# Kernel optimization log

Measured on AMD Instinct MI355X. Metric: run time of the kernel, lower is better.

## Reference

```python
import jax, jax.numpy as jnp
import numpy as np
import math

B, S, D, H = 4, 2048, 1024, 16
HD = D // H  # head dim = 64


def setup_inputs() -> dict:
    key = jax.random.key(0)
    ks = jax.random.split(key, 8)
    queries = jax.random.normal(ks[0], (B, S, D), dtype=jnp.float32)
    keys = jax.random.normal(ks[1], (B, S, D), dtype=jnp.float32)
    values = jax.random.normal(ks[2], (B, S, D), dtype=jnp.float32)
    valid_lens = jnp.maximum(jax.random.randint(ks[3], (B,), 0, S), 1).astype(jnp.int64)
    scale = 1.0 / math.sqrt(D)
    Wq = jax.random.normal(ks[4], (H, D, HD), dtype=jnp.float32) * scale
    Wk = jax.random.normal(ks[5], (H, D, HD), dtype=jnp.float32) * scale
    Wv = jax.random.normal(ks[6], (H, D, HD), dtype=jnp.float32) * scale
    Wo = jax.random.normal(ks[7], (H * HD, D), dtype=jnp.float32) * scale
    return {"queries": queries, "keys": keys, "values": values,
            "valid_lens": valid_lens, "Wq": Wq, "Wk": Wk, "Wv": Wv, "Wo": Wo}


def reference(queries, keys, values, valid_lens, Wq, Wk, Wv, Wo):
    # Per-head projections, batched over heads: [B,S,D] x [H,D,HD] -> [B,H,S,HD]
    q = jnp.einsum('bsd,hde->bhse', queries, Wq)
    k = jnp.einsum('bsd,hde->bhse', keys, Wk)
    v = jnp.einsum('bsd,hde->bhse', values, Wv)
    # Scaled dot-product scores: [B,H,S,S]
    scores = jnp.einsum('bhse,bhte->bhst', q, k) / jnp.sqrt(jnp.float32(HD))
    # Padding mask only (causal=False default in the torch forward)
    pad = jnp.arange(S)[None, :] >= valid_lens[:, None]  # [B,S] True = masked
    scores = jnp.where(pad[:, None, None, :], -jnp.inf, scores)
    attn = jax.nn.softmax(scores, axis=-1)
    out = jnp.einsum('bhst,bhte->bhse', attn, v)  # [B,H,S,HD]
    out = out.transpose(0, 2, 1, 3).reshape(q.shape[0], S, H * HD)  # concat heads
    return out @ Wo
```

## Files before the change

### kernel.cpp

```cpp
#include <hip/hip_runtime.h>
#include <hip/hip_bf16.h>

typedef __bf16 bf16;
typedef __attribute__((ext_vector_type(8))) __bf16 bf16x8;
typedef __attribute__((ext_vector_type(4))) float f32x4;

#define DEV __device__ __forceinline__

DEV float fexp2(float x) {
#if __has_builtin(__builtin_amdgcn_exp2f)
  return __builtin_amdgcn_exp2f(x);
#else
  return exp2f(x);
#endif
}

DEV void gload_lds16(const void* g, void* l) {
  __builtin_amdgcn_global_load_lds(
      (__attribute__((address_space(1))) void*)(g),
      (__attribute__((address_space(3))) void*)(l), 16, 0, 0);
}

template <int N>
DEV void waitvm() { asm volatile("s_waitcnt vmcnt(%0)" ::"n"(N) : "memory"); }
DEV void fence() { asm volatile("" ::: "memory"); }
DEV void bar() { fence(); __builtin_amdgcn_s_barrier(); fence(); }

__global__ void k_cvt_act(const float* __restrict__ q, const float* __restrict__ k,
                          const float* __restrict__ v, bf16* __restrict__ qb,
                          bf16* __restrict__ kb, bf16* __restrict__ vb) {
  const int bid = blockIdx.x;
  const int which = bid >> 12;
  const float* in = which == 0 ? q : which == 1 ? k : v;
  bf16* out = which == 0 ? qb : which == 1 ? kb : vb;
  const int i = (bid & 4095) * 256 + threadIdx.x;
  const float4* p = reinterpret_cast<const float4*>(in) + (size_t)i * 2;
  float4 a = p[0], b = p[1];
  bf16x8 o;
  o[0] = (bf16)a.x; o[1] = (bf16)a.y; o[2] = (bf16)a.z; o[3] = (bf16)a.w;
  o[4] = (bf16)b.x; o[5] = (bf16)b.y; o[6] = (bf16)b.z; o[7] = (bf16)b.w;
  *reinterpret_cast<bf16x8*>(out + (size_t)i * 8) = o;
}

__global__ void k_cvt_w(const float* __restrict__ Wq, const float* __restrict__ Wk,
                        const float* __restrict__ Wv, const float* __restrict__ Wo,
                        bf16* __restrict__ WqkvT, bf16* __restrict__ WoT) {
  const int idx = blockIdx.x * blockDim.x + threadIdx.x;
  const int which = idx >> 20, r = idx & ((1 << 20) - 1);
  if (which < 3) {
    const float* W = which == 0 ? Wq : which == 1 ? Wk : Wv;
    const int d = r & 1023, n = r >> 10;
    float val = W[((size_t)(n >> 6) << 16) + (size_t)d * 64 + (n & 63)];
    if (which == 0) val *= 0.180336880f;
    WqkvT[((size_t)which << 20) + r] = (bf16)val;
  } else {
    const int kk = r & 1023, n = r >> 10;
    WoT[r] = (bf16)Wo[(size_t)kk * 1024 + n];
  }
}

DEV void stage_half(const bf16* __restrict__ srcb, bf16 (*lds)[64], int h, int k0,
                    int tid) {
  const int wv = tid >> 6;
#pragma unroll
  for (int l = 0; l < 2; ++l) {
    const int row = h * 128 + l * 64 + (tid >> 3);
    const int e = (((tid & 7) ^ (row & 7)) << 3);
    gload_lds16(srcb + (size_t)row * 1024 + k0 + e,
                (char*)&lds[h * 128 + l * 64][0] + wv * 1024);
  }
}

DEV bf16x8 ldsfrag(const bf16 (*lds)[64], int row, int kk, int lgrp) {
  const int ch = ((kk << 2) + lgrp) ^ (row & 7);
  return *reinterpret_cast<const bf16x8*>((const char*)&lds[row][0] + (ch << 4));
}

__global__ __launch_bounds__(512, 2) void k_gemm_qkv(const bf16* __restrict__ qA,
                                                     const bf16* __restrict__ kA,
                                                     const bf16* __restrict__ vA,
                                                     const bf16* __restrict__ Wt,
                                                     bf16* __restrict__ Qh,
                                                     bf16* __restrict__ Kh,
                                                     bf16* __restrict__ Vt) {
  __shared__ __align__(16) bf16 AsB[2][256][64];
  __shared__ __align__(16) bf16 BsB[2][256][64];
  const int tid = threadIdx.x, lane = tid & 63, w = tid >> 6;
  const int lgrp = lane >> 4, lid = lane & 15;
  const int wr = w >> 2, wn = w & 3;
  const int bid0 = blockIdx.x;
  const int bid = (bid0 & 7) * 48 + (bid0 >> 3);
  const int proj = bid >> 7;
  const int rem = bid & 127;
  const int mt = rem >> 2, ntl = rem & 3;
  const int m0 = mt * 256, n0 = ntl * 256;
  const bf16* A = proj == 0 ? qA : proj == 1 ? kA : vA;
  const bf16* Am = A + (size_t)m0 * 1024;
  const bf16* Bt = Wt + ((size_t)proj * 1024 + n0) * 1024;

  f32x4 acc[8][4] = {};
  constexpr int NT = 16;

  stage_half(Am, AsB[0], 0, 0, tid);
  stage_half(Am, AsB[0], 1, 0, tid);
  stage_half(Bt, BsB[0], 0, 0, tid);
  stage_half(Bt, BsB[0], 1, 0, tid);
  stage_half(Bt, BsB[1], 0, 64, tid);
  stage_half(Bt, BsB[1], 1, 64, tid);
  waitvm<4>();
  bar();

  int cur = 0;
  for (int kt = 0; kt < NT; ++kt) {
    bf16x8 bfr[4][2];
#pragma unroll
    for (int p = 0; p < 4; ++p) {
      if (p == 0) {
#pragma unroll
        for (int n = 0; n < 4; ++n)
#pragma unroll
          for (int kk = 0; kk < 2; ++kk)
            bfr[n][kk] = ldsfrag(BsB[cur], wn * 64 + n * 16 + lid, kk, lgrp);
      }
      bf16x8 afr[2][2];
#pragma unroll
      for (int mi = 0; mi < 2; ++mi)
#pragma unroll
        for (int kk = 0; kk < 2; ++kk)
          afr[mi][kk] = ldsfrag(AsB[cur], wr * 128 + (p * 2 + mi) * 16 + lid, kk, lgrp);
      if (p < 2) {
        if (kt + 1 < NT) stage_half(Am, AsB[cur ^ 1], p, (kt + 1) * 64, tid);
      } else {
        if (kt + 2 < NT) stage_half(Bt, BsB[cur], p - 2, (kt + 2) * 64, tid);
      }
      bar();
      __builtin_amdgcn_s_setprio(1);
#pragma unroll
      for (int mi = 0; mi < 2; ++mi)
#pragma unroll
        for (int n = 0; n < 4; ++n)
#pragma unroll
          for (int kk = 0; kk < 2; ++kk)
            acc[p * 2 + mi][n] = __builtin_amdgcn_mfma_f32_16x16x32_bf16(
                afr[mi][kk], bfr[n][kk], acc[p * 2 + mi][n], 0, 0, 0);
      __builtin_amdgcn_s_setprio(0);
      if (p == 3) {
        if (kt < NT - 2) waitvm<4>();
        else if (kt == NT - 2) waitvm<0>();
      }
      bar();
    }
    cur ^= 1;
  }

  const int hh = (n0 >> 6) + wn;
  if (proj == 0) {
#pragma unroll
    for (int mm = 0; mm < 8; ++mm) {
      const int rowb = m0 + wr * 128 + mm * 16 + lgrp * 4;
      const int bb = rowb >> 11, s = rowb & 2047;
#pragma unroll
      for (int n = 0; n < 4; ++n) {
        const int e = n * 16 + lid;
        bf16* dst = Qh + (((size_t)bb * 16 + hh) * 2048 + s) * 64 + e;
#pragma unroll
        for (int r = 0; r < 4; ++r) dst[(size_t)r * 64] = (bf16)acc[mm][n][r];
      }
    }
  } else if (proj == 1) {
#pragma unroll
    for (int mm = 0; mm < 8; ++mm) {
      const int rowb = m0 + wr * 128 + mm * 16 + lgrp * 4;
      const int bb = rowb >> 11, s = rowb & 2047;
#pragma unroll
      for (int n = 0; n < 4; ++n) {
        const int e = n * 16 + lid;
#pragma unroll
        for (int r = 0; r < 4; ++r) {
          const int sr = s + r;
          Kh[(((size_t)bb * 16 + hh) * 2048 + sr) * 64 + (e ^ ((sr & 7) << 3))] =
              (bf16)acc[mm][n][r];
        }
      }
    }
  } else {
#pragma unroll
    for (int mm = 0; mm < 8; ++mm) {
      const int rowb = m0 + wr * 128 + mm * 16 + lgrp * 4;
      const int bb = rowb >> 11, s = rowb & 2047;
#pragma unroll
      for (int n = 0; n < 4; ++n) {
        const int e = n * 16 + lid;
        union { bf16 hv[4]; uint2 u; } tmp;
#pragma unroll
        for (int r = 0; r < 4; ++r) tmp.hv[r] = (bf16)acc[mm][n][r];
        bf16* dst = Vt + (((size_t)bb * 16 + hh) * 64 + e) * 2048 + (s ^ ((e & 7) << 3));
        *reinterpret_cast<uint2*>(dst) = tmp.u;
      }
    }
  }
}

__global__ __launch_bounds__(256) void k_gemm_out(const bf16* __restrict__ A,
                                                  const bf16* __restrict__ Bt,
                                                  float* __restrict__ C) {
  constexpr int K = 1024;
  __shared__ __align__(16) bf16 As[128 * 32];
  __shared__ __align__(16) bf16 Bs[128 * 32];
  const int tid = threadIdx.x;
  const int lane = tid & 63, w = tid >> 6;
  const int wr = w >> 1, wc = w & 1;
  const int lgrp = lane >> 4, lid = lane & 15;
  const int m0 = blockIdx.x * 128, n0 = blockIdx.y * 128;

  f32x4 acc[4][4] = {};
  const int c0 = w * 2, c1 = w * 2 + 1;
  const int bo0 = c0 * 1024 + lane * 16, bo1 = c1 * 1024 + lane * 16;
  const int r0 = bo0 >> 6, e0 = (bo0 & 63) >> 1;
  const int r1 = bo1 >> 6, e1 = (bo1 & 63) >> 1;

  for (int k0 = 0; k0 < K; k0 += 32) {
    __syncthreads();
    gload_lds16(A + (size_t)(m0 + r0) * K + k0 + e0, (char*)As + c0 * 1024);
    gload_lds16(A + (size_t)(m0 + r1) * K + k0 + e1, (char*)As + c1 * 1024);
    gload_lds16(Bt + (size_t)(n0 + r0) * K + k0 + e0, (char*)Bs + c0 * 1024);
    gload_lds16(Bt + (size_t)(n0 + r1) * K + k0 + e1, (char*)Bs + c1 * 1024);
    __syncthreads();
    bf16x8 af[4], bfv[4];
    for (int m = 0; m < 4; ++m)
      af[m] = *reinterpret_cast<const bf16x8*>(&As[(wr * 64 + m * 16 + lid) * 32 + lgrp * 8]);
    for (int n = 0; n < 4; ++n)
      bfv[n] = *reinterpret_cast<const bf16x8*>(&Bs[(wc * 64 + n * 16 + lid) * 32 + lgrp * 8]);
    for (int m = 0; m < 4; ++m)
      for (int n = 0; n < 4; ++n)
        acc[m][n] = __builtin_amdgcn_mfma_f32_16x16x32_bf16(af[m], bfv[n], acc[m][n], 0, 0, 0);
  }
  for (int m = 0; m < 4; ++m) {
    int rowb = m0 + wr * 64 + m * 16 + lgrp * 4;
    for (int n = 0; n < 4; ++n) {
      int col = n0 + wc * 64 + n * 16 + lid;
      for (int r = 0; r < 4; ++r)
        C[(size_t)(rowb + r) * 1024 + col] = acc[m][n][r];
    }
  }
}

__global__ __launch_bounds__(512) void k_flash(const bf16* __restrict__ Qh,
                                               const bf16* __restrict__ Ksw,
                                               const bf16* __restrict__ Vsw,
                                               const int* __restrict__ valid,
                                               bf16* __restrict__ Ob) {
  __shared__ __align__(16) char Ks[2][64 * 128];
  __shared__ __align__(16) char Vs[2][64 * 128];
  __shared__ __align__(16) char Plds[8][16 * 128];
  const int tid = threadIdx.x, lane = tid & 63, w = tid >> 6;
  const int lgrp = lane >> 4, lid = lane & 15;
  const int blk = blockIdx.x;
  const int qt = blk & 15, bh = blk >> 4;
  const int b = bh >> 4, h = bh & 15;
  const int s0 = qt * 128 + w * 16;
  const bf16* Qp = Qh + ((size_t)bh * 2048 + s0) * 64;
  const bf16* Kp = Ksw + (size_t)bh * 2048 * 64;
  const bf16* Vp = Vsw + (size_t)bh * 64 * 2048;
  const int vl = valid[b];
  const int nt = (vl + 63) >> 6;
  const int full = vl >> 6;

  const int srow = 8 * w + (lane >> 3), col8 = (lane & 7) * 8;

  gload_lds16(Kp + (size_t)srow * 64 + col8, &Ks[0][(8 * w) * 128]);
  gload_lds16(Vp + (size_t)srow * 2048 + col8, &Vs[0][(8 * w) * 128]);

  bf16x8 aq0 = *reinterpret_cast<const bf16x8*>(Qp + lid * 64 + lgrp * 8);
  bf16x8 aq1 = *reinterpret_cast<const bf16x8*>(Qp + lid * 64 + 32 + lgrp * 8);

  f32x4 Of[4] = {};
  float mrow = -1e30f;
  float lpart = 0.f;
  char* Pw = &Plds[w][0];
  float* PwF = (float*)Pw;
  const int pswz = (lid & 7) << 4;

  int cur = 0;
  for (int t = 0; t < nt; ++t) {
    const int t0 = t * 64;
    __syncthreads();
    if (t + 1 < nt) {
      const int t1 = t0 + 64;
      gload_lds16(Kp + (size_t)(t1 + srow) * 64 + col8, &Ks[cur ^ 1][(8 * w) * 128]);
      gload_lds16(Vp + (size_t)srow * 2048 + t1 + col8, &Vs[cur ^ 1][(8 * w) * 128]);
    }
    f32x4 sc[4] = {};
#pragma unroll
    for (int ct = 0; ct < 4; ++ct) {
      const int row = ct * 16 + lid;
      const char* kb = &Ks[cur][row * 128];
      const int msk = (row & 7) << 4;
      bf16x8 bk0 = *reinterpret_cast<const bf16x8*>(kb + ((lgrp * 16) ^ msk));
      bf16x8 bk1 = *reinterpret_cast<const bf16x8*>(kb + ((64 + lgrp * 16) ^ msk));
      sc[ct] = __builtin_amdgcn_mfma_f32_16x16x32_bf16(bk0, aq0, sc[ct], 0, 0, 0);
      sc[ct] = __builtin_amdgcn_mfma_f32_16x16x32_bf16(bk1, aq1, sc[ct], 0, 0, 0);
    }
    if (t >= full) {
#pragma unroll
      for (int ct = 0; ct < 4; ++ct)
#pragma unroll
        for (int r = 0; r < 4; ++r)
          sc[ct][r] = (t0 + ct * 16 + lgrp * 4 + r) >= vl ? -1e30f : sc[ct][r];
    }
    float vm = fmaxf(fmaxf(fmaxf(sc[0][0], sc[0][1]), fmaxf(sc[0][2], sc[0][3])),
                     fmaxf(fmaxf(sc[1][0], sc[1][1]), fmaxf(sc[1][2], sc[1][3])));
    vm = fmaxf(vm, fmaxf(fmaxf(fmaxf(sc[2][0], sc[2][1]), fmaxf(sc[2][2], sc[2][3])),
                         fmaxf(fmaxf(sc[3][0], sc[3][1]), fmaxf(sc[3][2], sc[3][3]))));
    if (__any(vm > mrow + 8.f)) {
      vm = fmaxf(vm, __shfl_xor(vm, 16));
      vm = fmaxf(vm, __shfl_xor(vm, 32));
      float mnew = fmaxf(mrow, vm);
      float scl = fexp2(mrow - mnew);
      mrow = mnew;
      lpart *= scl;
      if (lgrp == 0) PwF[lid] = scl;
      asm volatile("s_waitcnt lgkmcnt(0)" ::: "memory");
      f32x4 sq = *reinterpret_cast<const f32x4*>(PwF + lgrp * 4);
#pragma unroll
      for (int f = 0; f < 4; ++f)
#pragma unroll
        for (int r = 0; r < 4; ++r)
          Of[f][r] *= sq[r];
    }
#pragma unroll
    for (int ct = 0; ct < 4; ++ct)
#pragma unroll
      for (int r = 0; r < 4; ++r)
        sc[ct][r] = fexp2(sc[ct][r] - mrow);
#pragma unroll
    for (int ct = 0; ct < 4; ++ct) {
      union { bf16 hv[2]; unsigned int u; } p0, p1;
      p0.hv[0] = (bf16)sc[ct][0]; p0.hv[1] = (bf16)sc[ct][1];
      p1.hv[0] = (bf16)sc[ct][2]; p1.hv[1] = (bf16)sc[ct][3];
      char* base = Pw + lid * 128 + (((ct * 32 + lgrp * 8)) ^ pswz);
      *reinterpret_cast<unsigned int*>(base) = p0.u;
      *reinterpret_cast<unsigned int*>(base + 4) = p1.u;
    }
    asm volatile("s_waitcnt lgkmcnt(0)" ::: "memory");
    bf16x8 pa0 = *reinterpret_cast<const bf16x8*>(Pw + lid * 128 + ((lgrp * 16) ^ pswz));
    bf16x8 pa1 = *reinterpret_cast<const bf16x8*>(Pw + lid * 128 + ((64 + lgrp * 16) ^ pswz));
#pragma unroll
    for (int f = 0; f < 4; ++f) {
      const int row = f * 16 + lid;
      const char* vb = &Vs[cur][row * 128];
      const int msk = (row & 7) << 4;
      bf16x8 bv0 = *reinterpret_cast<const bf16x8*>(vb + ((lgrp * 16) ^ msk));
      bf16x8 bv1 = *reinterpret_cast<const bf16x8*>(vb + ((64 + lgrp * 16) ^ msk));
      Of[f] = __builtin_amdgcn_mfma_f32_16x16x32_bf16(pa0, bv0, Of[f], 0, 0, 0);
      Of[f] = __builtin_amdgcn_mfma_f32_16x16x32_bf16(pa1, bv1, Of[f], 0, 0, 0);
    }
    lpart += ((sc[0][0] + sc[0][1]) + (sc[0][2] + sc[0][3])) +
             ((sc[1][0] + sc[1][1]) + (sc[1][2] + sc[1][3])) +
             ((sc[2][0] + sc[2][1]) + (sc[2][2] + sc[2][3])) +
             ((sc[3][0] + sc[3][1]) + (sc[3][2] + sc[3][3]));
    cur ^= 1;
  }
  float l = lpart;
  l += __shfl_xor(l, 16);
  l += __shfl_xor(l, 32);
  float inv = 1.f / l;
  if (lgrp == 0) PwF[lid] = inv;
  asm volatile("s_waitcnt lgkmcnt(0)" ::: "memory");
  f32x4 invq = *reinterpret_cast<const f32x4*>(PwF + lgrp * 4);
  bf16* Op = Ob + ((size_t)b * 2048 + s0) * 1024 + h * 64;
#pragma unroll
  for (int r = 0; r < 4; ++r)
#pragma unroll
    for (int f = 0; f < 4; ++f)
      Op[(size_t)(lgrp * 4 + r) * 1024 + f * 16 + lid] = (bf16)(Of[f][r] * invq[r]);
}

extern "C" void kernel_launch(void* const* d_in, const int* in_sizes, int n_in,
                              void* d_out, int out_size, void* d_ws, size_t ws_size,
                              hipStream_t stream) {
  const float* q = (const float*)d_in[0];
  const float* k = (const float*)d_in[1];
  const float* v = (const float*)d_in[2];
  const int* vl = (const int*)d_in[3];
  const float* Wq = (const float*)d_in[4];
  const float* Wk = (const float*)d_in[5];
  const float* Wv = (const float*)d_in[6];
  const float* Wo = (const float*)d_in[7];

  char* ws = (char*)d_ws;
  const size_t SZW = (size_t)1024 * 1024 * 2;
  const size_t SZT = (size_t)8192 * 1024 * 2;
  bf16* WqkvT = (bf16*)(ws);
  bf16* WoT = (bf16*)(ws + 3 * SZW);
  bf16* Qh  = (bf16*)(ws + 4 * SZW);
  bf16* Kh  = (bf16*)(ws + 4 * SZW + SZT);
  bf16* Vt  = (bf16*)(ws + 4 * SZW + 2 * SZT);
  bf16* qb  = (bf16*)(ws + 4 * SZW + 3 * SZT);
  bf16* kb  = (bf16*)(ws + 4 * SZW + 4 * SZT);
  bf16* vb  = (bf16*)(ws + 4 * SZW + 5 * SZT);
  bf16* attnb = qb;

  k_cvt_act<<<12288, 256, 0, stream>>>(q, k, v, qb, kb, vb);
  k_cvt_w<<<16384, 256, 0, stream>>>(Wq, Wk, Wv, Wo, WqkvT, WoT);
  k_gemm_qkv<<<384, 512, 0, stream>>>(qb, kb, vb, WqkvT, Qh, Kh, Vt);
  k_flash<<<1024, 512, 0, stream>>>(Qh, Kh, Vt, vl, attnb);
  dim3 go(64, 8);
  k_gemm_out<<<go, 256, 0, stream>>>(attnb, WoT, (float*)d_out);
}
```

Measured before the change: 212.2 us.

## Halve QKV GEMM M-tile to 128 rows and double grid size

Shrinks the QKV projection GEMM block tile from 256x256 to 128x256, doubling the grid to 768 blocks and halving A-tile LDS and accumulator registers. The K-loop is restructured into two half-phases, one prefetching the next A tile and one the B tile two steps ahead. This aims to fix wave quantization and improve occupancy, at the cost of reloading B tiles twice as often.

```diff
diff --git a/kernel.cpp b/kernel.cpp
--- a/kernel.cpp
+++ b/kernel.cpp
@@ -59,15 +59,24 @@
   }
 }
 
-DEV void stage_half(const bf16* __restrict__ srcb, bf16 (*lds)[64], int h, int k0,
-                    int tid) {
+DEV void stageA(const bf16* __restrict__ Am, bf16 (*lds)[64], int k0, int tid) {
+  const int wv = tid >> 6;
+#pragma unroll
+  for (int l = 0; l < 2; ++l) {
+    const int row = l * 64 + (tid >> 3);
+    const int e = (((tid & 7) ^ (row & 7)) << 3);
+    gload_lds16(Am + (size_t)row * 1024 + k0 + e,
+                (char*)lds + l * 8192 + wv * 1024);
+  }
+}
+DEV void stageBh(const bf16* __restrict__ Bt, bf16 (*lds)[64], int h, int k0, int tid) {
   const int wv = tid >> 6;
 #pragma unroll
   for (int l = 0; l < 2; ++l) {
     const int row = h * 128 + l * 64 + (tid >> 3);
     const int e = (((tid & 7) ^ (row & 7)) << 3);
-    gload_lds16(srcb + (size_t)row * 1024 + k0 + e,
-                (char*)&lds[h * 128 + l * 64][0] + wv * 1024);
+    gload_lds16(Bt + (size_t)row * 1024 + k0 + e,
+                (char*)lds + h * 16384 + l * 8192 + wv * 1024);
   }
 }
 
@@ -83,81 +92,89 @@
                                                      bf16* __restrict__ Qh,
                                                      bf16* __restrict__ Kh,
                                                      bf16* __restrict__ Vt) {
-  __shared__ __align__(16) bf16 AsB[2][256][64];
+  __shared__ __align__(16) bf16 AsB[2][128][64];
   __shared__ __align__(16) bf16 BsB[2][256][64];
   const int tid = threadIdx.x, lane = tid & 63, w = tid >> 6;
   const int lgrp = lane >> 4, lid = lane & 15;
   const int wr = w >> 2, wn = w & 3;
   const int bid0 = blockIdx.x;
-  const int bid = (bid0 & 7) * 48 + (bid0 >> 3);
-  const int proj = bid >> 7;
-  const int rem = bid & 127;
-  const int mt = rem >> 2, ntl = rem & 3;
-  const int m0 = mt * 256, n0 = ntl * 256;
+  const int bid = (bid0 & 7) * 96 + (bid0 >> 3);
+  const int proj = bid >> 8;
+  const int local = bid & 255;
+  const int mt = local >> 2, ntl = local & 3;
+  const int m0 = mt * 128, n0 = ntl * 256;
   const bf16* A = proj == 0 ? qA : proj == 1 ? kA : vA;
   const bf16* Am = A + (size_t)m0 * 1024;
   const bf16* Bt = Wt + ((size_t)proj * 1024 + n0) * 1024;
 
-  f32x4 acc[8][4] = {};
+  f32x4 acc[4][4] = {};
   constexpr int NT = 16;
 
-  stage_half(Am, AsB[0], 0, 0, tid);
-  stage_half(Am, AsB[0], 1, 0, tid);
-  stage_half(Bt, BsB[0], 0, 0, tid);
-  stage_half(Bt, BsB[0], 1, 0, tid);
-  stage_half(Bt, BsB[1], 0, 64, tid);
-  stage_half(Bt, BsB[1], 1, 64, tid);
+  stageA(Am, AsB[0], 0, tid);
+  stageBh(Bt, BsB[0], 0, 0, tid);
+  stageBh(Bt, BsB[0], 1, 0, tid);
+  stageBh(Bt, BsB[1], 0, 64, tid);
+  stageBh(Bt, BsB[1], 1, 64, tid);
   waitvm<4>();
   bar();
 
   int cur = 0;
   for (int kt = 0; kt < NT; ++kt) {
-    bf16x8 bfr[4][2];
-#pragma unroll
-    for (int p = 0; p < 4; ++p) {
-      if (p == 0) {
-#pragma unroll
-        for (int n = 0; n < 4; ++n)
-#pragma unroll
-          for (int kk = 0; kk < 2; ++kk)
-            bfr[n][kk] = ldsfrag(BsB[cur], wn * 64 + n * 16 + lid, kk, lgrp);
-      }
-      bf16x8 afr[2][2];
-#pragma unroll
-      for (int mi = 0; mi < 2; ++mi)
+    bf16x8 bfr[4][2], afr[2][2];
+#pragma unroll
+    for (int n = 0; n < 4; ++n)
+#pragma unroll
+      for (int kk = 0; kk < 2; ++kk)
+        bfr[n][kk] = ldsfrag(BsB[cur], wn * 64 + n * 16 + lid, kk, lgrp);
+#pragma unroll
+    for (int mi = 0; mi < 2; ++mi)
+#pragma unroll
+      for (int kk = 0; kk < 2; ++kk)
+        afr[mi][kk] = ldsfrag(AsB[cur], wr * 64 + mi * 16 + lid, kk, lgrp);
+    if (kt + 1 < NT) stageA(Am, AsB[cur ^ 1], (kt + 1) * 64, tid);
+    bar();
+    __builtin_amdgcn_s_setprio(1);
+#pragma unroll
+    for (int mi = 0; mi < 2; ++mi)
+#pragma unroll
+      for (int n = 0; n < 4; ++n)
 #pragma unroll
         for (int kk = 0; kk < 2; ++kk)
-          afr[mi][kk] = ldsfrag(AsB[cur], wr * 128 + (p * 2 + mi) * 16 + lid, kk, lgrp);
-      if (p < 2) {
-        if (kt + 1 < NT) stage_half(Am, AsB[cur ^ 1], p, (kt + 1) * 64, tid);
-      } else {
-        if (kt + 2 < NT) stage_half(Bt, BsB[cur], p - 2, (kt + 2) * 64, tid);
-      }
-      bar();
-      __builtin_amdgcn_s_setprio(1);
-#pragma unroll
-      for (int mi = 0; mi < 2; ++mi)
-#pragma unroll
-        for (int n = 0; n < 4; ++n)
-#pragma unroll
-          for (int kk = 0; kk < 2; ++kk)
-            acc[p * 2 + mi][n] = __builtin_amdgcn_mfma_f32_16x16x32_bf16(
-                afr[mi][kk], bfr[n][kk], acc[p * 2 + mi][n], 0, 0, 0);
-      __builtin_amdgcn_s_setprio(0);
-      if (p == 3) {
-        if (kt < NT - 2) waitvm<4>();
-        else if (kt == NT - 2) waitvm<0>();
-      }
-      bar();
-    }
+          acc[mi][n] = __builtin_amdgcn_mfma_f32_16x16x32_bf16(
+              afr[mi][kk], bfr[n][kk], acc[mi][n], 0, 0, 0);
+    __builtin_amdgcn_s_setprio(0);
+    bar();
+#pragma unroll
+    for (int mi = 0; mi < 2; ++mi)
+#pragma unroll
+      for (int kk = 0; kk < 2; ++kk)
+        afr[mi][kk] = ldsfrag(AsB[cur], wr * 64 + (2 + mi) * 16 + lid, kk, lgrp);
+    if (kt + 2 < NT) {
+      stageBh(Bt, BsB[cur], 0, (kt + 2) * 64, tid);
+      stageBh(Bt, BsB[cur], 1, (kt + 2) * 64, tid);
+    }
+    bar();
+    __builtin_amdgcn_s_setprio(1);
+#pragma unroll
+    for (int mi = 0; mi < 2; ++mi)
+#pragma unroll
+      for (int n = 0; n < 4; ++n)
+#pragma unroll
+        for (int kk = 0; kk < 2; ++kk)
+          acc[2 + mi][n] = __builtin_amdgcn_mfma_f32_16x16x32_bf16(
+              afr[mi][kk], bfr[n][kk], acc[2 + mi][n], 0, 0, 0);
+    __builtin_amdgcn_s_setprio(0);
+    if (kt < NT - 2) waitvm<4>();
+    else if (kt == NT - 2) waitvm<0>();
+    bar();
     cur ^= 1;
   }
 
   const int hh = (n0 >> 6) + wn;
   if (proj == 0) {
 #pragma unroll
-    for (int mm = 0; mm < 8; ++mm) {
-      const int rowb = m0 + wr * 128 + mm * 16 + lgrp * 4;
+    for (int mm = 0; mm < 4; ++mm) {
+      const int rowb = m0 + wr * 64 + mm * 16 + lgrp * 4;
       const int bb = rowb >> 11, s = rowb & 2047;
 #pragma unroll
       for (int n = 0; n < 4; ++n) {
@@ -169,8 +186,8 @@
     }
   } else if (proj == 1) {
 #pragma unroll
-    for (int mm = 0; mm < 8; ++mm) {
-      const int rowb = m0 + wr * 128 + mm * 16 + lgrp * 4;
+    for (int mm = 0; mm < 4; ++mm) {
+      const int rowb = m0 + wr * 64 + mm * 16 + lgrp * 4;
       const int bb = rowb >> 11, s = rowb & 2047;
 #pragma unroll
       for (int n = 0; n < 4; ++n) {
@@ -185,8 +202,8 @@
     }
   } else {
 #pragma unroll
-    for (int mm = 0; mm < 8; ++mm) {
-      const int rowb = m0 + wr * 128 + mm * 16 + lgrp * 4;
+    for (int mm = 0; mm < 4; ++mm) {
+      const int rowb = m0 + wr * 64 + mm * 16 + lgrp * 4;
       const int bb = rowb >> 11, s = rowb & 2047;
 #pragma unroll
       for (int n = 0; n < 4; ++n) {
@@ -403,7 +420,7 @@
 
   k_cvt_act<<<12288, 256, 0, stream>>>(q, k, v, qb, kb, vb);
   k_cvt_w<<<16384, 256, 0, stream>>>(Wq, Wk, Wv, Wo, WqkvT, WoT);
-  k_gemm_qkv<<<384, 512, 0, stream>>>(qb, kb, vb, WqkvT, Qh, Kh, Vt);
+  k_gemm_qkv<<<768, 512, 0, stream>>>(qb, kb, vb, WqkvT, Qh, Kh, Vt);
   k_flash<<<1024, 512, 0, stream>>>(Qh, Kh, Vt, vl, attnb);
   dim3 go(64, 8);
   k_gemm_out<<<go, 256, 0, stream>>>(attnb, WoT, (float*)d_out);
```

Measured after the change: 194.8 us. -8.2%, faster.
